# Optimization experiments

Measured on AMD Instinct MI355X. Metric: run time of the kernel, lower is better.

## Reference

```python
import jax, jax.numpy as jnp
import numpy as np

EMB = 1280
MD = 200
N = 20000
E = 200000
LN_EPS = 1e-5


def _layer_norm(x, g, b):
    mu = jnp.mean(x, axis=-1, keepdims=True)
    var = jnp.mean((x - mu) ** 2, axis=-1, keepdims=True)
    return (x - mu) * jax.lax.rsqrt(var + LN_EPS) * g + b


def _gat_conv(x, edge_index, edge_attr, W, We, a_src, a_dst, a_edge, bias, heads, C):
    """PyG GATConv (bias-free lin, edge_dim, add_self_loops with fill='mean')."""
    n = x.shape[0]
    src, dst = edge_index[0], edge_index[1]
    # self-loop edge_attr = mean of incoming edge_attr per dst node (0 if none)
    cnt = jax.ops.segment_sum(jnp.ones((edge_attr.shape[0],), x.dtype), dst, n)
    s = jax.ops.segment_sum(edge_attr, dst, n)
    loop_attr = jnp.where(cnt[:, None] > 0, s / jnp.maximum(cnt, 1.0)[:, None], 0.0)
    loop = jnp.arange(n)
    src = jnp.concatenate([src, loop])
    dst = jnp.concatenate([dst, loop])
    ea = jnp.concatenate([edge_attr, loop_attr], axis=0)
    h = (x @ W).reshape(n, heads, C)                      # [N,H,C]
    al_s = jnp.einsum('nhc,hc->nh', h, a_src)
    al_d = jnp.einsum('nhc,hc->nh', h, a_dst)
    eh = (ea @ We).reshape(-1, heads, C)                  # [E+N,H,C]
    al_e = jnp.einsum('ehc,hc->eh', eh, a_edge)
    alpha = jax.nn.leaky_relu(al_s[src] + al_d[dst] + al_e, 0.2)
    amax = jax.ops.segment_max(alpha, dst, n)
    amax = jnp.where(jnp.isfinite(amax), amax, 0.0)
    ex = jnp.exp(alpha - amax[dst])
    denom = jax.ops.segment_sum(ex, dst, n)
    w = ex / (denom[dst] + 1e-16)                         # segment softmax over dst
    out = jax.ops.segment_sum(h[src] * w[:, :, None], dst, n)
    return out.reshape(n, heads * C) + bias


def _forward(x, edge_index, edge_attr,
             ca_qw, ca_qb, ca_kw, ca_kb, ca_vw, ca_vb, ca_ow, ca_ob,
             g0_w, g0_ew, g0_as, g0_ad, g0_ae, g0_b, ln0_g, ln0_b,
             g1_w, g1_ew, g1_as, g1_ad, g1_ae, g1_b, ln1_g, ln1_b,
             g2_w, g2_ew, g2_as, g2_ad, g2_ae, g2_b, ln2_g, ln2_b,
             cls_w1, cls_b1, cls_w2, cls_b2):
    xe = x[:, :EMB]
    md = x[0, EMB:]
    # CrossAttention: single md vector -> K,V are [1,hidden]
    Q = xe @ ca_qw + ca_qb                                # [N,hid]
    K = md @ ca_kw + ca_kb                                # [hid]
    V = md @ ca_vw + ca_vb                                # [hid]
    scores = (Q @ K) / jnp.sqrt(jnp.asarray(Q.shape[-1], Q.dtype))  # [N]
    wts = jax.nn.softmax(scores, axis=0)[:, None]         # softmax over nodes
    attended = wts * V[None, :]                           # [N,hid]
    h = attended @ ca_ow + ca_ob + xe                     # [N,EMB]

    h = _gat_conv(h, edge_index, edge_attr, g0_w, g0_ew, g0_as, g0_ad, g0_ae, g0_b, 4, 256)
    h = jax.nn.relu(_layer_norm(h, ln0_g, ln0_b))
    h = _gat_conv(h, edge_index, edge_attr, g1_w, g1_ew, g1_as, g1_ad, g1_ae, g1_b, 4, 256)
    h = jax.nn.relu(_layer_norm(h, ln1_g, ln1_b))
    h = _gat_conv(h, edge_index, edge_attr, g2_w, g2_ew, g2_as, g2_ad, g2_ae, g2_b, 1, 256)
    h = jax.nn.relu(_layer_norm(h, ln2_g, ln2_b))

    g = jnp.mean(h, axis=0, keepdims=True)                # [1,256]
    g = jax.nn.relu(g @ cls_w1 + cls_b1)
    return g @ cls_w2 + cls_b2                            # [1,2]


def setup_inputs() -> dict:
    key = jax.random.key(0)
    ks = jax.random.split(key, 64)
    i = [0]
    def nrm(shape, scale=0.05):
        i[0] += 1
        return jax.random.normal(ks[i[0]], shape, jnp.float32) * scale
    inp = {}
    inp['x'] = nrm((N, EMB + MD), 1.0)
    inp['edge_index'] = jax.random.randint(ks[60], (2, E), 0, N, jnp.int64 if jax.config.read('jax_enable_x64') else jnp.int32)
    inp['edge_attr'] = jax.random.uniform(ks[61], (E, 1), jnp.float32)
    inp.update(ca_qw=nrm((EMB, 256)), ca_qb=jnp.zeros((256,), jnp.float32),
               ca_kw=nrm((MD, 256)), ca_kb=jnp.zeros((256,), jnp.float32),
               ca_vw=nrm((MD, 256)), ca_vb=jnp.zeros((256,), jnp.float32),
               ca_ow=nrm((256, EMB)), ca_ob=jnp.zeros((EMB,), jnp.float32))
    inp.update(g0_w=nrm((EMB, 1024)), g0_ew=nrm((1, 1024)), g0_as=nrm((4, 256)),
               g0_ad=nrm((4, 256)), g0_ae=nrm((4, 256)), g0_b=jnp.zeros((1024,), jnp.float32),
               ln0_g=jnp.ones((1024,), jnp.float32), ln0_b=jnp.zeros((1024,), jnp.float32))
    inp.update(g1_w=nrm((1024, 1024)), g1_ew=nrm((1, 1024)), g1_as=nrm((4, 256)),
               g1_ad=nrm((4, 256)), g1_ae=nrm((4, 256)), g1_b=jnp.zeros((1024,), jnp.float32),
               ln1_g=jnp.ones((1024,), jnp.float32), ln1_b=jnp.zeros((1024,), jnp.float32))
    inp.update(g2_w=nrm((1024, 256)), g2_ew=nrm((1, 256)), g2_as=nrm((1, 256)),
               g2_ad=nrm((1, 256)), g2_ae=nrm((1, 256)), g2_b=jnp.zeros((256,), jnp.float32),
               ln2_g=jnp.ones((256,), jnp.float32), ln2_b=jnp.zeros((256,), jnp.float32))
    inp.update(cls_w1=nrm((256, 128)), cls_b1=jnp.zeros((128,), jnp.float32),
               cls_w2=nrm((128, 2)), cls_b2=jnp.zeros((2,), jnp.float32))
    return inp


def reference(x, edge_index, edge_attr,
              ca_qw, ca_qb, ca_kw, ca_kb, ca_vw, ca_vb, ca_ow, ca_ob,
              g0_w, g0_ew, g0_as, g0_ad, g0_ae, g0_b, ln0_g, ln0_b,
              g1_w, g1_ew, g1_as, g1_ad, g1_ae, g1_b, ln1_g, ln1_b,
              g2_w, g2_ew, g2_as, g2_ad, g2_ae, g2_b, ln2_g, ln2_b,
              cls_w1, cls_b1, cls_w2, cls_b2):
    return _forward(x, edge_index, edge_attr,
                    ca_qw, ca_qb, ca_kw, ca_kb, ca_vw, ca_vb, ca_ow, ca_ob,
                    g0_w, g0_ew, g0_as, g0_ad, g0_ae, g0_b, ln0_g, ln0_b,
                    g1_w, g1_ew, g1_as, g1_ad, g1_ae, g1_b, ln1_g, ln1_b,
                    g2_w, g2_ew, g2_as, g2_ad, g2_ae, g2_b, ln2_g, ln2_b,
                    cls_w1, cls_b1, cls_w2, cls_b2)
```

## Files before the change

### kernel.cpp

```cpp
#include <hip/hip_runtime.h>
#include <hip/hip_bf16.h>
#include <math.h>

#define N_NODES 20000
#define N_EDGES 200000
#define XROW    1480

typedef __attribute__((ext_vector_type(8))) _Float16 f16x8;
typedef __attribute__((ext_vector_type(8))) unsigned short u16x8;
typedef __attribute__((ext_vector_type(4))) float f32x4v;

__device__ __forceinline__ float wsum(float v){
#pragma unroll
  for (int o=32;o>0;o>>=1) v += __shfl_down(v,o);
  return v;
}
__device__ __forceinline__ float wmax(float v){
#pragma unroll
  for (int o=32;o>0;o>>=1) v = fmaxf(v,__shfl_down(v,o));
  return v;
}
__device__ __forceinline__ float wsum_all(float v){
#pragma unroll
  for (int o=32;o>0;o>>=1) v += __shfl_xor(v,o);
  return v;
}
__device__ __forceinline__ float wmax_all(float v){
#pragma unroll
  for (int o=32;o>0;o>>=1) v = fmaxf(v,__shfl_xor(v,o));
  return v;
}

__device__ __forceinline__ unsigned short f2hu(float f){
  _Float16 h = (_Float16)f;
  return __builtin_bit_cast(unsigned short, h);
}
__device__ __forceinline__ float hu2f(unsigned short u){
  return (float)__builtin_bit_cast(_Float16, u);
}

__device__ __forceinline__ void async_copy16(void* lds, const void* g){
  __builtin_amdgcn_global_load_lds((const __attribute__((address_space(1))) void*)g,
                                   (__attribute__((address_space(3))) void*)lds, 16, 0, 0);
}

__global__ void edge_count_kernel(const int* __restrict__ ei, const float* __restrict__ ea,
                                  int* __restrict__ cnt, float* __restrict__ easum, int E){
  int e = blockIdx.x*256 + threadIdx.x;
  if (e >= E) return;
  int dst = ei[E + e];
  atomicAdd(&cnt[dst], 1);
  atomicAdd(&easum[dst], ea[e]);
}

__launch_bounds__(1024)
__global__ void scan_kernel(const int* __restrict__ cnt, const float* __restrict__ easum,
                            int* __restrict__ off, float* __restrict__ loop_attr, int n){
  __shared__ int buf[1024];
  const int PER = (N_NODES + 1023)/1024;
  int t = threadIdx.x;
  int base = t*PER;
  int local[PER];
  int s = 0;
#pragma unroll
  for (int k=0;k<PER;k++){
    int i = base + k;
    int v = (i<n)? cnt[i] : 0;
    local[k] = v;
    s += v;
  }
  buf[t] = s;
  __syncthreads();
  for (int d2=1; d2<1024; d2<<=1){
    int tv = (t>=d2)? buf[t-d2] : 0;
    __syncthreads();
    buf[t] += tv;
    __syncthreads();
  }
  int run = buf[t] - s;
#pragma unroll
  for (int k=0;k<PER;k++){
    int i = base + k;
    if (i < n){
      off[i] = run;
      int v = local[k];
      loop_attr[i] = (v>0) ? easum[i]/(float)v : 0.f;
      run += v;
    }
  }
  if (t == 1023) off[n] = buf[1023];
}

__global__ void edge_fill_kernel(const int* __restrict__ ei, const float* __restrict__ ea,
                                 const int* __restrict__ off, int* __restrict__ fill,
                                 int* __restrict__ csr_src, float* __restrict__ csr_ea, int E){
  int e = blockIdx.x*256 + threadIdx.x;
  if (e >= E) return;
  int dst = ei[E + e];
  int pos = off[dst] + atomicAdd(&fill[dst], 1);
  csr_src[pos] = ei[e];
  csr_ea[pos]  = ea[e];
}

__global__ void x_to_f16(const float* __restrict__ x, unsigned short* __restrict__ xh){
  const int CH4 = 1280/4;
  long total = (long)N_NODES*CH4;
  for (long i = (long)blockIdx.x*256 + threadIdx.x; i < total; i += (long)gridDim.x*256){
    int row = (int)(i / CH4), c4 = (int)(i % CH4);
    float4 v = *(const float4*)(x + (size_t)row*XROW + c4*4);
    ushort4 o;
    o.x = f2hu(v.x); o.y = f2hu(v.y); o.z = f2hu(v.z); o.w = f2hu(v.w);
    *(ushort4*)(xh + (size_t)row*1280 + c4*4) = o;
  }
}

__global__ void wt_f16_kernel(const float* __restrict__ W, int K, int N,
                              unsigned short* __restrict__ Wt){
  __shared__ float tile[32][33];
  int k0 = blockIdx.x*32, n0 = blockIdx.y*32;
  int tx = threadIdx.x & 31, ty = threadIdx.x >> 5;
  for (int r=ty; r<32; r+=8) tile[r][tx] = W[(size_t)(k0+r)*N + n0+tx];
  __syncthreads();
  for (int r=ty; r<32; r+=8){
    float w = tile[tx][r];
    Wt[(size_t)(n0+r)*K + k0+tx] = f2hu(w);
  }
}

__global__ void kv_kernel(const float* __restrict__ x,
                          const float* __restrict__ kw, const float* __restrict__ kb,
                          const float* __restrict__ vw, const float* __restrict__ vb,
                          float* __restrict__ Kv, float* __restrict__ Vv){
  int j = threadIdx.x;
  float ka = kb[j], va = vb[j];
  for (int k=0;k<200;k++){
    float m = x[1280+k];
    ka = fmaf(m, kw[k*256+j], ka);
    va = fmaf(m, vw[k*256+j], va);
  }
  Kv[j]=ka; Vv[j]=va;
}

__global__ void qkvo_kernel(const float* __restrict__ qw, const float* __restrict__ ow,
                            const float* __restrict__ Kv, const float* __restrict__ Vv,
                            float* __restrict__ qK, float* __restrict__ Vo){
  int idx = blockIdx.x*256 + threadIdx.x;
  if (idx < 1280){
    float a=0;
    for (int j=0;j<256;j++) a = fmaf(qw[idx*256+j], Kv[j], a);
    qK[idx]=a;
  } else if (idx < 2560){
    int j = idx-1280;
    float a=0;
    for (int i=0;i<256;i++) a = fmaf(Vv[i], ow[(size_t)i*1280+j], a);
    Vo[j]=a;
  }
}

__global__ void obw_kernel(const float* __restrict__ ob, const float* __restrict__ Vo,
                           const float* __restrict__ W, float* __restrict__ obW, float* __restrict__ VoW){
  int j = blockIdx.x*256 + threadIdx.x;
  float a=0,b=0;
  for (int i=0;i<1280;i++){
    float w = W[(size_t)i*1024+j];
    a = fmaf(ob[i], w, a);
    b = fmaf(Vo[i], w, b);
  }
  obW[j]=a; VoW[j]=b;
}

__launch_bounds__(256)
__global__ void scores_kernel(const unsigned short* __restrict__ xh, const float* __restrict__ qK,
                              float* __restrict__ scores, int n){
  __shared__ float qs[1280];
  int t = threadIdx.x;
  for (int i=t;i<1280;i+=256) qs[i]=qK[i];
  __syncthreads();
  int wid = t>>6, lane = t&63;
  int node = blockIdx.x*4 + wid;
  if (node >= n) return;
  const u16x8* row = (const u16x8*)(xh + (size_t)node*1280);
  float acc = 0;
#pragma unroll
  for (int it=0; it<3; it++){
    int chunk = it*64 + lane;
    if (chunk < 160){
      u16x8 v = row[chunk];
#pragma unroll
      for (int k=0;k<8;k++) acc = fmaf(hu2f(v[k]), qs[chunk*8+k], acc);
    }
  }
  acc = wsum(acc);
  if (lane==0) scores[node] = acc;
}

__launch_bounds__(1024)
__global__ void softmax_nodes(const float* __restrict__ scores, float* __restrict__ wts, int n){
  __shared__ float red[16];
  int t = threadIdx.x, lane=t&63, wid=t>>6;
  float m = -INFINITY;
  for (int i=t;i<n;i+=1024) m = fmaxf(m, scores[i]);
  m = wmax(m);
  if (lane==0) red[wid]=m;
  __syncthreads();
  if (t==0){ float r=red[0]; for (int k=1;k<16;k++) r=fmaxf(r,red[k]); red[0]=r; }
  __syncthreads();
  float M = red[0];
  __syncthreads();
  float z=0;
  for (int i=t;i<n;i+=1024) z += expf((scores[i]-M)*(1.f/16.f));
  z = wsum(z);
  if (lane==0) red[wid]=z;
  __syncthreads();
  if (t==0){ float r=0; for (int k=0;k<16;k++) r+=red[k]; red[0]=r; }
  __syncthreads();
  float invZ = 1.f/red[0];
  for (int i=t;i<n;i+=1024) wts[i] = expf((scores[i]-M)*(1.f/16.f))*invZ;
}

__launch_bounds__(256)
__global__ void gemm_f16(const unsigned short* __restrict__ A,
                         const unsigned short* __restrict__ B,
                         unsigned short* __restrict__ C, int M, int N, int K,
                         const float* __restrict__ addCol,
                         const float* __restrict__ vCol,
                         const float* __restrict__ wRow,
                         const float* __restrict__ a_src,
                         const float* __restrict__ a_dst,
                         float* __restrict__ alsp,
                         float* __restrict__ aldp)
{
  __shared__ short lds[2*128*64];
  short* As = lds;
  short* Bs = lds + 128*64;

  const int ntc = N >> 7;
  const int sh  = __popc(ntc - 1);
  const int g   = blockIdx.y >> sh;
  const int nt  = blockIdx.y & (ntc - 1);
  const int band = blockIdx.x + (g << 3);
  if (band * 128 >= M) return;

  const int t = threadIdx.x;
  const int w = t>>6, l = t&63;
  const int bm = band*128, bn = nt*128;
  const int wr = (w>>1)*64, wc = (w&1)*64;
  const int half = w & 1;

  f32x4v acc[4][4];
#pragma unroll
  for (int i=0;i<4;i++)
#pragma unroll
    for (int j=0;j<4;j++) acc[i][j] = (f32x4v){0.f,0.f,0.f,0.f};

  const unsigned short* Ap[4]; const unsigned short* Bp[4];
  int ldsOff[4];
#pragma unroll
  for (int q=0;q<4;q++){
    int p  = (w*4+q)*64 + l;
    int r  = p>>3, pc = p&7;
    int kc = (pc ^ (r&7))*8;
    int rowA = bm + r; if (rowA > M-1) rowA = M-1;
    Ap[q] = A + (size_t)rowA*K + kc;
    Bp[q] = B + (size_t)(bn+r)*K + kc;
    ldsOff[q] = (w*4+q)*64*8;
  }

  for (int k0=0; k0<K; k0+=64){
#pragma unroll
    for (int q=0;q<4;q++) async_copy16(As + ldsOff[q], Ap[q] + k0);
#pragma unroll
    for (int q=0;q<4;q++) async_copy16(Bs + ldsOff[q], Bp[q] + k0);
    __syncthreads();

    const int q4 = l>>4, m16 = l&15;
#pragma unroll
    for (int ks=0; ks<2; ks++){
      f16x8 af[4], bf[4];
      const int c = ks*4 + q4;
#pragma unroll
      for (int i=0;i<4;i++){
        int ra = wr + i*16 + m16;
        af[i] = *(const f16x8*)&As[ra*64 + ((c ^ (ra&7))*8)];
        int rb = wc + i*16 + m16;
        bf[i] = *(const f16x8*)&Bs[rb*64 + ((c ^ (rb&7))*8)];
      }
#pragma unroll
      for (int i=0;i<4;i++)
#pragma unroll
        for (int j=0;j<4;j++)
          acc[i][j] = __builtin_amdgcn_mfma_f32_16x16x32_f16(af[i], bf[j], acc[i][j], 0,0,0);
    }
    __syncthreads();
  }

  float* sred = (float*)lds;
  float* dred = sred + 256;
  const int q4 = l>>4, m16 = l&15;
  float asv[4], adv[4];
#pragma unroll
  for (int j=0;j<4;j++){
    int n = bn + wc + j*16 + m16;
    asv[j] = a_src[n];
    adv[j] = a_dst[n];
  }
#pragma unroll
  for (int i=0;i<4;i++){
#pragma unroll
    for (int r=0;r<4;r++){
      int rloc = wr + i*16 + q4*4 + r;
      int m = bm + rloc;
      float wrow = addCol ? wRow[m < M ? m : M-1] : 0.f;
      float vj[4];
#pragma unroll
      for (int j=0;j<4;j++){
        int n = bn + wc + j*16 + m16;
        float v = acc[i][j][r];
        if (addCol) v += addCol[n] + wrow*vCol[n];
        vj[j] = v;
      }
      if (m < M){
        unsigned short* crow = C + (size_t)m*N;
#pragma unroll
        for (int j=0;j<4;j++) crow[bn + wc + j*16 + m16] = f2hu(vj[j]);
      }
      float s = vj[0]*asv[0] + vj[1]*asv[1] + vj[2]*asv[2] + vj[3]*asv[3];
      float d = vj[0]*adv[0] + vj[1]*adv[1] + vj[2]*adv[2] + vj[3]*adv[3];
#pragma unroll
      for (int o=1;o<16;o<<=1){ s += __shfl_xor(s,o); d += __shfl_xor(d,o); }
      if (m16 == 0){
        sred[half*128 + rloc] = s;
        dred[half*128 + rloc] = d;
      }
    }
  }
  __syncthreads();
  if (t < 128){
    int m = bm + t;
    if (m < M){
      alsp[(size_t)nt*M + m] = sred[t] + sred[128+t];
      aldp[(size_t)nt*M + m] = dred[t] + dred[128+t];
    }
  }
}

__global__ void als_combine(const float* __restrict__ alsp, const float* __restrict__ aldp,
                            float* __restrict__ als, float* __restrict__ ald, int M, int H){
  int idx = blockIdx.x*256 + threadIdx.x;
  if (idx >= M*H) return;
  int m = idx / H, hh = idx - m*H;
  als[idx] = alsp[(size_t)(2*hh)*M + m] + alsp[(size_t)(2*hh+1)*M + m];
  ald[idx] = aldp[(size_t)(2*hh)*M + m] + aldp[(size_t)(2*hh+1)*M + m];
}

template<int H>
__global__ void we_kernel(const float* __restrict__ We, const float* __restrict__ a_edge,
                          float* __restrict__ we){
  int wid = threadIdx.x>>6, lane = threadIdx.x&63;
  if (wid < H){
    const float4* w4 = (const float4*)(We + wid*256);
    const float4* a4 = (const float4*)(a_edge + wid*256);
    float4 a = w4[lane], b = a4[lane];
    float v = a.x*b.x + a.y*b.y + a.z*b.z + a.w*b.w;
    v = wsum(v);
    if (lane==0) we[wid]=v;
  }
}

template<int H>
__launch_bounds__(256)
__global__ void gat_agg_ln_wave(const unsigned short* __restrict__ hmat,
                           const float* __restrict__ als, const float* __restrict__ ald,
                           const int* __restrict__ off, const int* __restrict__ csr_src,
                           const float* __restrict__ csr_ea, const float* __restrict__ loop_attr,
                           const float* __restrict__ we,
                           const float* __restrict__ bias,
                           const float* __restrict__ ln_g, const float* __restrict__ ln_b,
                           float* __restrict__ outf, unsigned short* __restrict__ outb, int n)
{
  constexpr int OUT = 256*H;
  constexpr int CPL = OUT/64;
  const int wv = threadIdx.x>>6, lane = threadIdx.x&63;
  const int i = blockIdx.x*4 + wv;
  __shared__ float wbuf_s[4][64*H];
  __shared__ int   sbuf_s[4][64];
  if (i >= n) return;
  float* wbuf = wbuf_s[wv];
  int*   sbuf = sbuf_s[wv];

  const int begin = off[i];
  const int deg   = off[i+1]-begin;
  const int S     = deg + 1;

  float aldi[H], wei[H];
#pragma unroll
  for (int hh=0;hh<H;hh++){ aldi[hh]=ald[(size_t)i*H+hh]; wei[hh]=we[hh]; }
  const float lea = loop_attr[i];

  const int head = (lane*CPL) >> 8;
  const int c0   = lane*CPL;
  float acc[CPL];
#pragma unroll
  for (int c=0;c<CPL;c++) acc[c]=0.f;

  if (S <= 64){
    int src = i; float ev = lea;
    if (lane < deg){ src = csr_src[begin+lane]; ev = csr_ea[begin+lane]; }
    const bool act = lane < S;
    float a[H];
#pragma unroll
    for (int hh=0;hh<H;hh++){
      float v = als[(size_t)src*H+hh] + aldi[hh] + ev*wei[hh];
      a[hh] = v>0.f ? v : 0.2f*v;
    }
#pragma unroll
    for (int hh=0;hh<H;hh++){
      float M = wmax_all(act ? a[hh] : -INFINITY);
      float e = act ? __expf(a[hh]-M) : 0.f;
      float Z = wsum_all(e);
      wbuf[lane*H+hh] = e / (Z + 1e-16f);
    }
    sbuf[lane] = src;
    for (int j=0;j<S;j++){
      int sj = sbuf[j];
      float wj = wbuf[j*H+head];
      const unsigned short* row = hmat + (size_t)sj*OUT + c0;
      if constexpr (CPL==16){
        u16x8 r0 = *(const u16x8*)(row);
        u16x8 r1 = *(const u16x8*)(row+8);
#pragma unroll
        for (int c=0;c<8;c++){
          acc[c]   = fmaf(wj, hu2f(r0[c]), acc[c]);
          acc[8+c] = fmaf(wj, hu2f(r1[c]), acc[8+c]);
        }
      } else {
        ushort4 r = *(const ushort4*)(row);
        acc[0]=fmaf(wj,hu2f(r.x),acc[0]); acc[1]=fmaf(wj,hu2f(r.y),acc[1]);
        acc[2]=fmaf(wj,hu2f(r.z),acc[2]); acc[3]=fmaf(wj,hu2f(r.w),acc[3]);
      }
    }
  } else {
    float rm[H];
#pragma unroll
    for (int hh=0;hh<H;hh++) rm[hh] = -INFINITY;
    for (int s=lane; s<S; s+=64){
      int src = (s<deg)? csr_src[begin+s] : i;
      float ev = (s<deg)? csr_ea[begin+s] : lea;
#pragma unroll
      for (int hh=0;hh<H;hh++){
        float v = als[(size_t)src*H+hh] + aldi[hh] + ev*wei[hh];
        v = v>0.f? v : 0.2f*v;
        rm[hh] = fmaxf(rm[hh], v);
      }
    }
    float M[H], es[H];
#pragma unroll
    for (int hh=0;hh<H;hh++){ M[hh]=wmax_all(rm[hh]); es[hh]=0.f; }
    for (int s=lane; s<S; s+=64){
      int src = (s<deg)? csr_src[begin+s] : i;
      float ev = (s<deg)? csr_ea[begin+s] : lea;
#pragma unroll
      for (int hh=0;hh<H;hh++){
        float v = als[(size_t)src*H+hh] + aldi[hh] + ev*wei[hh];
        v = v>0.f? v : 0.2f*v;
        es[hh] += __expf(v - M[hh]);
      }
    }
    float invZ[H];
#pragma unroll
    for (int hh=0;hh<H;hh++) invZ[hh] = 1.f/(wsum_all(es[hh]) + 1e-16f);
    for (int cb=0; cb<S; cb+=64){
      int m = min(64, S-cb);
      int s = cb + lane;
      if (s < S){
        int src = (s<deg)? csr_src[begin+s] : i;
        float ev = (s<deg)? csr_ea[begin+s] : lea;
        sbuf[lane] = src;
#pragma unroll
        for (int hh=0;hh<H;hh++){
          float v = als[(size_t)src*H+hh] + aldi[hh] + ev*wei[hh];
          v = v>0.f? v : 0.2f*v;
          wbuf[lane*H+hh] = __expf(v - M[hh]) * invZ[hh];
        }
      }
      for (int j=0;j<m;j++){
        int sj = sbuf[j];
        float wj = wbuf[j*H+head];
        const unsigned short* row = hmat + (size_t)sj*OUT + c0;
        if constexpr (CPL==16){
          u16x8 r0 = *(const u16x8*)(row);
          u16x8 r1 = *(const u16x8*)(row+8);
#pragma unroll
          for (int c=0;c<8;c++){
            acc[c]   = fmaf(wj, hu2f(r0[c]), acc[c]);
            acc[8+c] = fmaf(wj, hu2f(r1[c]), acc[8+c]);
          }
        } else {
          ushort4 r = *(const ushort4*)(row);
          acc[0]=fmaf(wj,hu2f(r.x),acc[0]); acc[1]=fmaf(wj,hu2f(r.y),acc[1]);
          acc[2]=fmaf(wj,hu2f(r.z),acc[2]); acc[3]=fmaf(wj,hu2f(r.w),acc[3]);
        }
      }
    }
  }

  float vals[CPL];
  float ls=0.f;
#pragma unroll
  for (int c=0;c<CPL;c+=4){
    float4 b4 = *(const float4*)(bias + c0 + c);
    vals[c]=acc[c]+b4.x; vals[c+1]=acc[c+1]+b4.y; vals[c+2]=acc[c+2]+b4.z; vals[c+3]=acc[c+3]+b4.w;
    ls += vals[c]+vals[c+1]+vals[c+2]+vals[c+3];
  }
  float mu = wsum_all(ls) * (1.f/OUT);
  float lv=0.f;
#pragma unroll
  for (int c=0;c<CPL;c++){ float d=vals[c]-mu; lv += d*d; }
  float inv = rsqrtf(wsum_all(lv)*(1.f/OUT) + 1e-5f);

  if (outb){
    if constexpr (CPL==16){
#pragma unroll
      for (int c=0;c<CPL;c+=8){
        u16x8 o;
#pragma unroll
        for (int k=0;k<8;k++){
          float g = ln_g[c0+c+k], b = ln_b[c0+c+k];
          o[k] = f2hu(fmaxf((vals[c+k]-mu)*inv*g + b, 0.f));
        }
        *(u16x8*)(outb + (size_t)i*OUT + c0 + c) = o;
      }
    } else {
      ushort4 o;
      o.x = f2hu(fmaxf((vals[0]-mu)*inv*ln_g[c0+0] + ln_b[c0+0], 0.f));
      o.y = f2hu(fmaxf((vals[1]-mu)*inv*ln_g[c0+1] + ln_b[c0+1], 0.f));
      o.z = f2hu(fmaxf((vals[2]-mu)*inv*ln_g[c0+2] + ln_b[c0+2], 0.f));
      o.w = f2hu(fmaxf((vals[3]-mu)*inv*ln_g[c0+3] + ln_b[c0+3], 0.f));
      *(ushort4*)(outb + (size_t)i*OUT + c0) = o;
    }
  } else {
#pragma unroll
    for (int c=0;c<CPL;c+=4){
      float4 g4 = *(const float4*)(ln_g + c0 + c);
      float4 b4 = *(const float4*)(ln_b + c0 + c);
      float4 o;
      o.x = fmaxf((vals[c+0]-mu)*inv*g4.x + b4.x, 0.f);
      o.y = fmaxf((vals[c+1]-mu)*inv*g4.y + b4.y, 0.f);
      o.z = fmaxf((vals[c+2]-mu)*inv*g4.z + b4.z, 0.f);
      o.w = fmaxf((vals[c+3]-mu)*inv*g4.w + b4.w, 0.f);
      *(float4*)(outf + (size_t)i*OUT + c0 + c) = o;
    }
  }
}

__global__ void colsum_kernel(const float* __restrict__ h2, float* __restrict__ gsum, int n){
  int c = threadIdx.x;
  float acc=0;
  for (int i=blockIdx.x;i<n;i+=gridDim.x) acc += h2[(size_t)i*256 + c];
  atomicAdd(&gsum[c], acc);
}

__launch_bounds__(128)
__global__ void cls_kernel(const float* __restrict__ gsum,
                           const float* __restrict__ w1, const float* __restrict__ b1,
                           const float* __restrict__ w2, const float* __restrict__ b2,
                           float* __restrict__ outp){
  __shared__ float g[256];
  __shared__ float hid[128];
  int t = threadIdx.x;
  g[t]     = gsum[t]    *(1.f/N_NODES);
  g[t+128] = gsum[t+128]*(1.f/N_NODES);
  __syncthreads();
  float a = b1[t];
  for (int c=0;c<256;c++) a = fmaf(g[c], w1[c*128+t], a);
  hid[t] = fmaxf(a, 0.f);
  __syncthreads();
  if (t<2){
    float o = b2[t];
    for (int j=0;j<128;j++) o = fmaf(hid[j], w2[j*2+t], o);
    outp[t] = o;
  }
}

extern "C" void kernel_launch(void* const* d_in, const int* in_sizes, int n_in,
                              void* d_out, int out_size, void* d_ws, size_t ws_size,
                              hipStream_t stream)
{
  const float* x      = (const float*)d_in[0];
  const int*   ei     = (const int*)  d_in[1];
  const float* ea     = (const float*)d_in[2];
  const float* ca_qw  = (const float*)d_in[3];
  const float* ca_kw  = (const float*)d_in[5];
  const float* ca_kb  = (const float*)d_in[6];
  const float* ca_vw  = (const float*)d_in[7];
  const float* ca_vb  = (const float*)d_in[8];
  const float* ca_ow  = (const float*)d_in[9];
  const float* ca_ob  = (const float*)d_in[10];
  const float* g0_w   = (const float*)d_in[11];
  const float* g0_ew  = (const float*)d_in[12];
  const float* g0_as  = (const float*)d_in[13];
  const float* g0_ad  = (const float*)d_in[14];
  const float* g0_ae  = (const float*)d_in[15];
  const float* g0_b   = (const float*)d_in[16];
  const float* ln0_g  = (const float*)d_in[17];
  const float* ln0_b  = (const float*)d_in[18];
  const float* g1_w   = (const float*)d_in[19];
  const float* g1_ew  = (const float*)d_in[20];
  const float* g1_as  = (const float*)d_in[21];
  const float* g1_ad  = (const float*)d_in[22];
  const float* g1_ae  = (const float*)d_in[23];
  const float* g1_b   = (const float*)d_in[24];
  const float* ln1_g  = (const float*)d_in[25];
  const float* ln1_b  = (const float*)d_in[26];
  const float* g2_w   = (const float*)d_in[27];
  const float* g2_ew  = (const float*)d_in[28];
  const float* g2_as  = (const float*)d_in[29];
  const float* g2_ad  = (const float*)d_in[30];
  const float* g2_ae  = (const float*)d_in[31];
  const float* g2_b   = (const float*)d_in[32];
  const float* ln2_g  = (const float*)d_in[33];
  const float* ln2_b  = (const float*)d_in[34];
  const float* cls_w1 = (const float*)d_in[35];
  const float* cls_b1 = (const float*)d_in[36];
  const float* cls_w2 = (const float*)d_in[37];
  const float* cls_b2 = (const float*)d_in[38];
  float* outp = (float*)d_out;

  const int N = N_NODES, E = N_EDGES;

  char* base = (char*)d_ws;
  size_t o = 0;
  auto alloc = [&](size_t bytes)->void*{
    void* p = base + o;
    o += (bytes + 255) & ~(size_t)255;
    return p;
  };
  unsigned short* hF   = (unsigned short*)alloc((size_t)N*1024*2);
  unsigned short* Af   = (unsigned short*)alloc((size_t)N*1280*2);
  float*          h2   = (float*)         alloc((size_t)N*256*4);
  unsigned short* Wt   = (unsigned short*)alloc((size_t)1280*1024*2);
  float* alsp      = (float*)alloc((size_t)8*N*4);
  float* aldp      = (float*)alloc((size_t)8*N*4);
  float* als       = (float*)alloc((size_t)2*N*4*4);
  float* ald       = als + (size_t)N*4;
  float* scores    = (float*)alloc((size_t)N*4);
  float* wts       = (float*)alloc((size_t)N*4);
  int*   cnt       = (int*)  alloc((size_t)N*4);
  float* easum     = (float*)alloc((size_t)N*4);
  int*   off       = (int*)  alloc((size_t)(N+1)*4);
  int*   fill      = (int*)  alloc((size_t)N*4);
  int*   csr_src   = (int*)  alloc((size_t)E*4);
  float* csr_ea    = (float*)alloc((size_t)E*4);
  float* loop_attr = (float*)alloc((size_t)N*4);
  float* Kv        = (float*)alloc(256*4);
  float* Vv        = (float*)alloc(256*4);
  float* qK        = (float*)alloc(1280*4);
  float* Vo        = (float*)alloc(1280*4);
  float* obW       = (float*)alloc(1024*4);
  float* VoW       = (float*)alloc(1024*4);
  float* web       = (float*)alloc(16*4);
  float* gsum      = (float*)alloc(256*4);

  hipMemsetAsync(cnt,   0, (size_t)N*4, stream);
  hipMemsetAsync(easum, 0, (size_t)N*4, stream);
  hipMemsetAsync(fill,  0, (size_t)N*4, stream);
  hipMemsetAsync(gsum,  0, 256*4,       stream);

  int eblocks = (E + 255)/256;
  edge_count_kernel<<<eblocks,256,0,stream>>>(ei, ea, cnt, easum, E);
  scan_kernel<<<1,1024,0,stream>>>(cnt, easum, off, loop_attr, N);
  edge_fill_kernel<<<eblocks,256,0,stream>>>(ei, ea, off, fill, csr_src, csr_ea, E);

  x_to_f16<<<2048,256,0,stream>>>(x, Af);

  kv_kernel<<<1,256,0,stream>>>(x, ca_kw, ca_kb, ca_vw, ca_vb, Kv, Vv);
  qkvo_kernel<<<10,256,0,stream>>>(ca_qw, ca_ow, Kv, Vv, qK, Vo);
  obw_kernel<<<4,256,0,stream>>>(ca_ob, Vo, g0_w, obW, VoW);
  scores_kernel<<<(N+3)/4,256,0,stream>>>(Af, qK, scores, N);
  softmax_nodes<<<1,1024,0,stream>>>(scores, wts, N);

  const int mTiles  = (N + 127)/128;
  const int mGroups = (mTiles + 7)/8;
  const int NB4 = (N + 3)/4;

  wt_f16_kernel<<<dim3(1280/32, 1024/32),256,0,stream>>>(g0_w, 1280, 1024, Wt);
  gemm_f16<<<dim3(8, mGroups*8),256,0,stream>>>(Af, Wt, hF, N, 1024, 1280, obW, VoW, wts,
                                                g0_as, g0_ad, alsp, aldp);
  als_combine<<<(N*4+255)/256,256,0,stream>>>(alsp, aldp, als, ald, N, 4);
  we_kernel<4><<<1,256,0,stream>>>(g0_ew, g0_ae, web);
  gat_agg_ln_wave<4><<<NB4,256,0,stream>>>(hF, als, ald, off, csr_src, csr_ea, loop_attr,
                                           web, g0_b, ln0_g, ln0_b, nullptr, Af, N);

  wt_f16_kernel<<<dim3(1024/32, 1024/32),256,0,stream>>>(g1_w, 1024, 1024, Wt);
  gemm_f16<<<dim3(8, mGroups*8),256,0,stream>>>(Af, Wt, hF, N, 1024, 1024, nullptr, nullptr, nullptr,
                                                g1_as, g1_ad, alsp, aldp);
  als_combine<<<(N*4+255)/256,256,0,stream>>>(alsp, aldp, als, ald, N, 4);
  we_kernel<4><<<1,256,0,stream>>>(g1_ew, g1_ae, web);
  gat_agg_ln_wave<4><<<NB4,256,0,stream>>>(hF, als, ald, off, csr_src, csr_ea, loop_attr,
                                           web, g1_b, ln1_g, ln1_b, nullptr, Af, N);

  wt_f16_kernel<<<dim3(1024/32, 256/32),256,0,stream>>>(g2_w, 1024, 256, Wt);
  gemm_f16<<<dim3(8, mGroups*2),256,0,stream>>>(Af, Wt, hF, N, 256, 1024, nullptr, nullptr, nullptr,
                                                g2_as, g2_ad, alsp, aldp);
  als_combine<<<(N+255)/256,256,0,stream>>>(alsp, aldp, als, ald, N, 1);
  we_kernel<1><<<1,256,0,stream>>>(g2_ew, g2_ae, web);
  gat_agg_ln_wave<1><<<NB4,256,0,stream>>>(hF, als, ald, off, csr_src, csr_ea, loop_attr,
                                           web, g2_b, ln2_g, ln2_b, h2, nullptr, N);

  colsum_kernel<<<256,256,0,stream>>>(h2, gsum, N);
  cls_kernel<<<1,128,0,stream>>>(gsum, cls_w1, cls_b1, cls_w2, cls_b2, outp);

  (void)in_sizes; (void)n_in; (void)out_size; (void)ws_size;
}
```

Baseline: 903.2 us.

## Double-buffer LDS tiles in the f16 GEMM to overlap global loads with MFMA

The GEMM mainloop now uses two LDS buffers and prefetches the next K-tile with async copies while the current tile feeds the MFMAs. It waits with an explicit vmcnt so only the older copies must land, and it raises wave priority around the MFMA block. The goal is to hide global-to-LDS latency that used to stall every iteration. The cost is doubled LDS (64KB per block), which may lower occupancy, and reliance on hand-placed waitcnt and barriers being correct.

```diff
diff --git a/kernel.cpp b/kernel.cpp
--- a/kernel.cpp
+++ b/kernel.cpp
@@ -230,9 +230,7 @@
                          float* __restrict__ alsp,
                          float* __restrict__ aldp)
 {
-  __shared__ short lds[2*128*64];
-  short* As = lds;
-  short* Bs = lds + 128*64;
+  __shared__ short lds[2*2*128*64];
 
   const int ntc = N >> 7;
   const int sh  = __popc(ntc - 1);
@@ -266,14 +264,34 @@
     ldsOff[q] = (w*4+q)*64*8;
   }
 
-  for (int k0=0; k0<K; k0+=64){
-#pragma unroll
-    for (int q=0;q<4;q++) async_copy16(As + ldsOff[q], Ap[q] + k0);
-#pragma unroll
-    for (int q=0;q<4;q++) async_copy16(Bs + ldsOff[q], Bp[q] + k0);
-    __syncthreads();
-
-    const int q4 = l>>4, m16 = l&15;
+  const int nsteps = K >> 6;
+
+#pragma unroll
+  for (int q=0;q<4;q++) async_copy16(lds + ldsOff[q],        Ap[q]);
+#pragma unroll
+  for (int q=0;q<4;q++) async_copy16(lds + 8192 + ldsOff[q], Bp[q]);
+
+  const int q4 = l>>4, m16 = l&15;
+
+  for (int ks0=0; ks0<nsteps; ++ks0){
+    short* curb = lds + (ks0&1)*16384;
+
+    if (ks0+1 < nsteps){
+      short* nxt = lds + ((ks0+1)&1)*16384;
+      const int k0n = (ks0+1)*64;
+#pragma unroll
+      for (int q=0;q<4;q++) async_copy16(nxt + ldsOff[q],        Ap[q] + k0n);
+#pragma unroll
+      for (int q=0;q<4;q++) async_copy16(nxt + 8192 + ldsOff[q], Bp[q] + k0n);
+      asm volatile("s_waitcnt vmcnt(8)" ::: "memory");
+    } else {
+      asm volatile("s_waitcnt vmcnt(0)" ::: "memory");
+    }
+    __builtin_amdgcn_sched_barrier(0);
+    __builtin_amdgcn_s_barrier();
+    __builtin_amdgcn_sched_barrier(0);
+
+    __builtin_amdgcn_s_setprio(1);
 #pragma unroll
     for (int ks=0; ks<2; ks++){
       f16x8 af[4], bf[4];
@@ -281,9 +299,9 @@
 #pragma unroll
       for (int i=0;i<4;i++){
         int ra = wr + i*16 + m16;
-        af[i] = *(const f16x8*)&As[ra*64 + ((c ^ (ra&7))*8)];
+        af[i] = *(const f16x8*)&curb[ra*64 + ((c ^ (ra&7))*8)];
         int rb = wc + i*16 + m16;
-        bf[i] = *(const f16x8*)&Bs[rb*64 + ((c ^ (rb&7))*8)];
+        bf[i] = *(const f16x8*)&curb[8192 + rb*64 + ((c ^ (rb&7))*8)];
       }
 #pragma unroll
       for (int i=0;i<4;i++)
@@ -291,12 +309,14 @@
         for (int j=0;j<4;j++)
           acc[i][j] = __builtin_amdgcn_mfma_f32_16x16x32_f16(af[i], bf[j], acc[i][j], 0,0,0);
     }
-    __syncthreads();
+    __builtin_amdgcn_s_setprio(0);
+    __builtin_amdgcn_sched_barrier(0);
+    __builtin_amdgcn_s_barrier();
+    __builtin_amdgcn_sched_barrier(0);
   }
 
   float* sred = (float*)lds;
   float* dred = sred + 256;
-  const int q4 = l>>4, m16 = l&15;
   float asv[4], adv[4];
 #pragma unroll
   for (int j=0;j<4;j++){
```

Result: faster. 862.6 us (-4.5%).
